# Performance work log

Measured on AMD Instinct MI355X. Metric: run time of the kernel, lower is better.

Reference implementation:

```python
import jax, jax.numpy as jnp
import numpy as np

B, T, C, HEAD = 8, 2048, 1024, 64


def setup_inputs() -> dict:
    key = jax.random.key(0)
    kx, kq, kk, kv = jax.random.split(key, 4)
    x = jax.random.normal(kx, (B, T, C), dtype=jnp.float32)
    Wq = jax.random.normal(kq, (C, HEAD), dtype=jnp.float32) * (C ** -0.5)
    Wk = jax.random.normal(kk, (C, HEAD), dtype=jnp.float32) * (C ** -0.5)
    Wv = jax.random.normal(kv, (C, HEAD), dtype=jnp.float32) * (C ** -0.5)
    return {"x": x, "Wq": Wq, "Wk": Wk, "Wv": Wv}


def reference(x, Wq, Wk, Wv):
    # q,k,v: [B, T, H] via bias-free linear projections
    q = jnp.einsum('btc,ch->bth', x, Wq)
    k = jnp.einsum('btc,ch->bth', x, Wk)
    v = jnp.einsum('btc,ch->bth', x, Wv)
    scale = k.shape[-1] ** -0.5
    # scores: [B, T, T]
    scores = jnp.einsum('bqh,bkh->bqk', q, k) * scale
    Tq = x.shape[1]
    causal = jnp.tril(jnp.ones((Tq, Tq), dtype=bool))  # [T, T]
    scores = jnp.where(causal[None, :, :], scores, -jnp.inf)
    # softmax forced to fp32 in the original (autocast block)
    weight = jax.nn.softmax(scores.astype(jnp.float32), axis=-1)
    # dropout is identity in eval / p=0 deterministic baseline
    out = jnp.einsum('bqk,bkh->bqh', weight.astype(v.dtype), v)  # [B, T, H]
    return out
```

## Files before the change

### kernel.cpp

```cpp
#include <hip/hip_runtime.h>
#include <hip/hip_bf16.h>
#include <stdint.h>

#define NB 8
#define NT 2048
#define NC 1024
#define NH 64

typedef __attribute__((ext_vector_type(8))) short bf16x8;
typedef __attribute__((ext_vector_type(4))) float f32x4;

#define MFMA(a, b, c) __builtin_amdgcn_mfma_f32_16x16x32_bf16((a), (b), (c), 0, 0, 0)

static __device__ __forceinline__ short f2bf(float f) {
  union { float f; uint32_t u; } v; v.f = f;
  uint32_t r = v.u + 0x7FFFu + ((v.u >> 16) & 1u);
  return (short)(r >> 16);
}
static __device__ __forceinline__ float bf2f(short h) {
  union { uint32_t u; float f; } v; v.u = ((uint32_t)(uint16_t)h) << 16;
  return v.f;
}
static __device__ __forceinline__ void gload_lds16(const void* g, void* l) {
  __builtin_amdgcn_global_load_lds(
      (const __attribute__((address_space(1))) uint32_t*)g,
      (__attribute__((address_space(3))) uint32_t*)l, 16, 0, 0);
}

__global__ __launch_bounds__(256) void w_prep(const float* __restrict__ Wq,
                                              const float* __restrict__ Wk,
                                              const float* __restrict__ Wv,
                                              short* __restrict__ Wt) {
  __shared__ short tile[64][68];
  const int blk = blockIdx.x;
  const int mat = blk / 16;
  const int k0 = (blk % 16) * 64;
  const float* W = (mat == 0) ? Wq : (mat == 1) ? Wk : Wv;
  const float scale = (mat == 0) ? 0.125f * 1.44269504088896f : 1.0f;
  const int tid = threadIdx.x;
  {
    int kk = tid >> 2;
    int h0 = (tid & 3) * 16;
    const float* src = W + (size_t)(k0 + kk) * NH + h0;
#pragma unroll
    for (int i = 0; i < 16; ++i) tile[kk][h0 + i] = f2bf(src[i] * scale);
  }
  __syncthreads();
  {
    int j = tid >> 2;
    int kk0 = (tid & 3) * 16;
    bf16x8 t0, t1;
#pragma unroll
    for (int i = 0; i < 8; ++i) { t0[i] = tile[kk0 + i][j]; t1[i] = tile[kk0 + 8 + i][j]; }
    short* dst = Wt + (size_t)(mat * 64 + j) * NC + k0 + kk0;
    *(bf16x8*)dst = t0;
    *(bf16x8*)(dst + 8) = t1;
  }
}

__global__ __launch_bounds__(512) void qkv_proj(const float* __restrict__ x,
                                                const short* __restrict__ Wt,
                                                short* __restrict__ Qo,
                                                short* __restrict__ Ko,
                                                short* __restrict__ VTo) {
  __shared__ char lds_raw[2][32768];
  const int tid = threadIdx.x;
  const int lane = tid & 63;
  const int wave = tid >> 6;
  const int l15 = lane & 15;
  const int hi = lane >> 4;
  const int m0 = blockIdx.x * 32;
  const int wr = wave & 1;
  const int wc = wave >> 1;

  f32x4 acc[3];
#pragma unroll
  for (int f = 0; f < 3; ++f) acc[f] = (f32x4){0.f, 0.f, 0.f, 0.f};

  int xr, xc;
  {
    int off = tid * 16;
    int ol = off ^ (((off >> 8) & 7) << 4);
    xr = ol >> 8; xc = (ol >> 2) & 63;
  }
  int wrow[3], wcol[3];
#pragma unroll
  for (int i = 0; i < 3; ++i) {
    int off = i * 8192 + tid * 16;
    int ol = off ^ (((off >> 7) & 7) << 4);
    wrow[i] = ol >> 7; wcol[i] = (ol >> 1) & 63;
  }

#define STAGE(k0, buf)                                                          \
  {                                                                             \
    char* xsb_ = lds_raw[buf];                                                  \
    char* wtb_ = lds_raw[buf] + 8192;                                           \
    gload_lds16(x + (size_t)(m0 + xr) * NC + (k0) + xc, xsb_ + tid * 16);       \
    _Pragma("unroll")                                                           \
    for (int i = 0; i < 3; ++i)                                                 \
      gload_lds16(Wt + (size_t)wrow[i] * NC + (k0) + wcol[i],                   \
                  wtb_ + i * 8192 + tid * 16);                                  \
  }

  STAGE(0, 0);
  __syncthreads();
  int cur = 0;
  for (int t = 0; t < 16; ++t) {
    if (t + 1 < 16) STAGE((t + 1) * 64, cur ^ 1);
    const char* xsb = lds_raw[cur];
    const char* wtb = lds_raw[cur] + 8192;
    const int r = wr * 16 + l15;
#pragma unroll
    for (int s = 0; s < 2; ++s) {
      int o1 = (r * 256 + s * 128 + hi * 32) ^ ((r & 7) << 4);
      int o2 = (r * 256 + s * 128 + hi * 32 + 16) ^ ((r & 7) << 4);
      float4 q0 = *(const float4*)(xsb + o1);
      float4 q1 = *(const float4*)(xsb + o2);
      bf16x8 a;
      a[0] = f2bf(q0.x); a[1] = f2bf(q0.y); a[2] = f2bf(q0.z); a[3] = f2bf(q0.w);
      a[4] = f2bf(q1.x); a[5] = f2bf(q1.y); a[6] = f2bf(q1.z); a[7] = f2bf(q1.w);
#pragma unroll
      for (int f = 0; f < 3; ++f) {
        int c = wc * 48 + f * 16 + l15;
        int ob = (c * 128 + s * 64 + hi * 16) ^ ((c & 7) << 4);
        bf16x8 b = *(const bf16x8*)(wtb + ob);
        acc[f] = MFMA(a, b, acc[f]);
      }
    }
    __syncthreads();
    cur ^= 1;
  }
#undef STAGE

#pragma unroll
  for (int f = 0; f < 3; ++f) {
    int c = wc * 48 + f * 16 + l15;
    int mat = c >> 6, h = c & 63;
    if (mat < 2) {
      short* dst = (mat == 0) ? Qo : Ko;
#pragma unroll
      for (int r = 0; r < 4; ++r) {
        int t = m0 + wr * 16 + hi * 4 + r;
        dst[(size_t)t * NH + h] = f2bf(acc[f][r]);
      }
    } else {
      int bb = m0 >> 11;
      int t0 = (m0 & 2047) + wr * 16 + hi * 4;
      short4 v;
      v.x = f2bf(acc[f][0]); v.y = f2bf(acc[f][1]);
      v.z = f2bf(acc[f][2]); v.w = f2bf(acc[f][3]);
      *(short4*)(VTo + ((size_t)(bb * 64 + h)) * NT + t0) = v;
    }
  }
}

__global__ __launch_bounds__(512, 2) void attn_fused(const short* __restrict__ Q,
                                                     const short* __restrict__ K,
                                                     const short* __restrict__ Vt,
                                                     float* __restrict__ out) {
  __shared__ short PO[8][32][72];
  __shared__ float Ls[8][32];

  const int tid = threadIdx.x;
  const int lane = tid & 63;
  const int wave = tid >> 6;
  const int l15 = lane & 15;
  const int hi = lane >> 4;
  const int kg = hi * 8;

  const int bid = blockIdx.x;
  const int half = bid >> 8;
  const int rr = bid & 255;
  const int b = rr >> 5;
  const int i = rr & 31;
  const int qt = (half == 0) ? (63 - i) : i;
  const int ktmax = qt >> 1;
  const int q0 = qt * 32;

  bf16x8 qf[2][2];
#pragma unroll
  for (int m = 0; m < 2; ++m)
#pragma unroll
    for (int s = 0; s < 2; ++s)
      qf[m][s] = *(const bf16x8*)(Q + ((size_t)b * NT + q0 + m * 16 + l15) * NH +
                                  s * 32 + kg);

  f32x4 oacc[2][4];
#pragma unroll
  for (int m = 0; m < 2; ++m)
#pragma unroll
    for (int f = 0; f < 4; ++f) oacc[m][f] = (f32x4){0.f, 0.f, 0.f, 0.f};
  float ps[2][4];
#pragma unroll
  for (int m = 0; m < 2; ++m)
#pragma unroll
    for (int r = 0; r < 4; ++r) ps[m][r] = 0.f;

#define LOAD_K(dst, kt_)                                                        \
  {                                                                             \
    const short* kb_ = K + ((size_t)b * NT + (kt_) * 64) * NH;                  \
    _Pragma("unroll") for (int n = 0; n < 4; ++n)                               \
    _Pragma("unroll") for (int s = 0; s < 2; ++s)                               \
      dst[n][s] = *(const bf16x8*)(kb_ + (n * 16 + l15) * NH + s * 32 + kg);    \
  }
#define LOAD_V(dst, kt_)                                                        \
  {                                                                             \
    _Pragma("unroll") for (int f = 0; f < 4; ++f)                               \
    _Pragma("unroll") for (int s = 0; s < 2; ++s)                               \
      dst[f][s] = *(const bf16x8*)(Vt + ((size_t)(b * 64 + f * 16 + l15)) * NT +\
                                   (kt_) * 64 + s * 32 + kg);                   \
  }

  int kt = wave;
  bf16x8 kf[4][2];
  if (kt <= ktmax) LOAD_K(kf, kt);

  for (; kt <= ktmax; kt += 8) {
    bf16x8 vf[4][2];
    LOAD_V(vf, kt);

    f32x4 S[2][4];
#pragma unroll
    for (int m = 0; m < 2; ++m)
#pragma unroll
      for (int n = 0; n < 4; ++n) {
        S[m][n] = (f32x4){0.f, 0.f, 0.f, 0.f};
        S[m][n] = MFMA(qf[m][0], kf[n][0], S[m][n]);
        S[m][n] = MFMA(qf[m][1], kf[n][1], S[m][n]);
      }

    bf16x8 kn[4][2];
    const bool more = (kt + 8) <= ktmax;
    if (more) LOAD_K(kn, kt + 8);

    if (kt == ktmax) {
#pragma unroll
      for (int m = 0; m < 2; ++m)
#pragma unroll
        for (int n = 0; n < 4; ++n)
#pragma unroll
          for (int r = 0; r < 4; ++r)
            if (kt * 64 + n * 16 + l15 > q0 + m * 16 + hi * 4 + r)
              S[m][n][r] = -INFINITY;
    }
#pragma unroll
    for (int m = 0; m < 2; ++m)
#pragma unroll
      for (int n = 0; n < 4; ++n)
#pragma unroll
        for (int r = 0; r < 4; ++r) {
          float p = __builtin_amdgcn_exp2f(S[m][n][r]);
          S[m][n][r] = p;
          ps[m][r] += p;
        }

#pragma unroll
    for (int m = 0; m < 2; ++m)
#pragma unroll
      for (int n = 0; n < 4; ++n)
#pragma unroll
        for (int r = 0; r < 4; ++r)
          PO[wave][m * 16 + hi * 4 + r][n * 16 + l15] = f2bf(S[m][n][r]);

    bf16x8 pa[2][2];
#pragma unroll
    for (int m = 0; m < 2; ++m)
#pragma unroll
      for (int s = 0; s < 2; ++s)
        pa[m][s] = *(const bf16x8*)&PO[wave][m * 16 + l15][s * 32 + kg];
#pragma unroll
    for (int m = 0; m < 2; ++m)
#pragma unroll
      for (int f = 0; f < 4; ++f) {
        oacc[m][f] = MFMA(pa[m][0], vf[f][0], oacc[m][f]);
        oacc[m][f] = MFMA(pa[m][1], vf[f][1], oacc[m][f]);
      }
    if (more) {
#pragma unroll
      for (int n = 0; n < 4; ++n)
#pragma unroll
        for (int s = 0; s < 2; ++s) kf[n][s] = kn[n][s];
    }
  }
#undef LOAD_K
#undef LOAD_V

#pragma unroll
  for (int d = 1; d < 16; d <<= 1)
#pragma unroll
    for (int m = 0; m < 2; ++m)
#pragma unroll
      for (int r = 0; r < 4; ++r) ps[m][r] += __shfl_xor(ps[m][r], d);

  if (l15 == 0) {
#pragma unroll
    for (int m = 0; m < 2; ++m)
#pragma unroll
      for (int r = 0; r < 4; ++r)
        Ls[wave][m * 16 + hi * 4 + r] = ps[m][r];
  }
#pragma unroll
  for (int m = 0; m < 2; ++m)
#pragma unroll
    for (int f = 0; f < 4; ++f)
#pragma unroll
      for (int r = 0; r < 4; ++r)
        PO[wave][m * 16 + hi * 4 + r][f * 16 + l15] = f2bf(oacc[m][f][r]);
  __syncthreads();

  {
    const int row = tid >> 4;
    const int c0 = (tid & 15) * 4;
    float L = 0.f;
    float o[4] = {0.f, 0.f, 0.f, 0.f};
#pragma unroll
    for (int w = 0; w < 8; ++w) {
      L += Ls[w][row];
      short4 v = *(const short4*)&PO[w][row][c0];
      o[0] += bf2f(v.x); o[1] += bf2f(v.y);
      o[2] += bf2f(v.z); o[3] += bf2f(v.w);
    }
    float inv = 1.f / L;
    float4 res = {o[0] * inv, o[1] * inv, o[2] * inv, o[3] * inv};
    *(float4*)(out + ((size_t)b * NT + q0 + row) * NH + c0) = res;
  }
}

extern "C" void kernel_launch(void* const* d_in, const int* in_sizes, int n_in,
                              void* d_out, int out_size, void* d_ws, size_t ws_size,
                              hipStream_t stream) {
  const float* x  = (const float*)d_in[0];
  const float* Wq = (const float*)d_in[1];
  const float* Wk = (const float*)d_in[2];
  const float* Wv = (const float*)d_in[3];
  float* out = (float*)d_out;

  char* ws = (char*)d_ws;
  short* Wt = (short*)ws;
  short* Qb = (short*)(ws + (size_t)(1 << 20));
  short* Kb = (short*)(ws + (size_t)(3 << 20));
  short* Vt = (short*)(ws + (size_t)(5 << 20));

  hipLaunchKernelGGL(w_prep, dim3(48), dim3(256), 0, stream, Wq, Wk, Wv, Wt);
  hipLaunchKernelGGL(qkv_proj, dim3(512), dim3(512), 0, stream, x, Wt, Qb, Kb, Vt);
  hipLaunchKernelGGL(attn_fused, dim3(512), dim3(512), 0, stream, Qb, Kb, Vt, out);
}
```

Baseline: 55.68 us.

## Shrink attention tile to 16 query rows with 4-wave blocks

New measurement: 61.02 us. +9.6%, slower.

```diff
diff --git a/kernel.cpp b/kernel.cpp
--- a/kernel.cpp
+++ b/kernel.cpp
@@ -154,12 +154,12 @@
   }
 }
 
-__global__ __launch_bounds__(512, 2) void attn_fused(const short* __restrict__ Q,
+__global__ __launch_bounds__(256, 4) void attn_fused(const short* __restrict__ Q,
                                                      const short* __restrict__ K,
                                                      const short* __restrict__ Vt,
                                                      float* __restrict__ out) {
-  __shared__ short PO[8][32][72];
-  __shared__ float Ls[8][32];
+  __shared__ short PO[4][16][72];
+  __shared__ float Ls[4][16];
 
   const int tid = threadIdx.x;
   const int lane = tid & 63;
@@ -169,143 +169,96 @@
   const int kg = hi * 8;
 
   const int bid = blockIdx.x;
-  const int half = bid >> 8;
-  const int rr = bid & 255;
-  const int b = rr >> 5;
-  const int i = rr & 31;
-  const int qt = (half == 0) ? (63 - i) : i;
-  const int ktmax = qt >> 1;
-  const int q0 = qt * 32;
-
-  bf16x8 qf[2][2];
-#pragma unroll
-  for (int m = 0; m < 2; ++m)
+  const int half = bid >> 9;
+  const int rr = bid & 511;
+  const int b = rr >> 6;
+  const int i = rr & 63;
+  const int qt = (half == 0) ? (127 - i) : i;
+  const int ktmax = qt >> 2;
+  const int q0 = qt * 16;
+
+  bf16x8 qf[2];
+#pragma unroll
+  for (int s = 0; s < 2; ++s)
+    qf[s] = *(const bf16x8*)(Q + ((size_t)b * NT + q0 + l15) * NH + s * 32 + kg);
+
+  f32x4 oacc[4];
+#pragma unroll
+  for (int f = 0; f < 4; ++f) oacc[f] = (f32x4){0.f, 0.f, 0.f, 0.f};
+  float ps[4];
+#pragma unroll
+  for (int r = 0; r < 4; ++r) ps[r] = 0.f;
+
+  for (int kt = wave; kt <= ktmax; kt += 4) {
+    const short* kb = K + ((size_t)b * NT + kt * 64) * NH;
+    bf16x8 kf[4][2], vf[4][2];
+#pragma unroll
+    for (int n = 0; n < 4; ++n)
+#pragma unroll
+      for (int s = 0; s < 2; ++s)
+        kf[n][s] = *(const bf16x8*)(kb + (n * 16 + l15) * NH + s * 32 + kg);
+#pragma unroll
+    for (int f = 0; f < 4; ++f)
+#pragma unroll
+      for (int s = 0; s < 2; ++s)
+        vf[f][s] = *(const bf16x8*)(Vt + ((size_t)(b * 64 + f * 16 + l15)) * NT +
+                                    kt * 64 + s * 32 + kg);
+
+    f32x4 S[4];
+#pragma unroll
+    for (int n = 0; n < 4; ++n) {
+      S[n] = (f32x4){0.f, 0.f, 0.f, 0.f};
+      S[n] = MFMA(qf[0], kf[n][0], S[n]);
+      S[n] = MFMA(qf[1], kf[n][1], S[n]);
+    }
+    if (kt == ktmax) {
+#pragma unroll
+      for (int n = 0; n < 4; ++n)
+#pragma unroll
+        for (int r = 0; r < 4; ++r)
+          if (kt * 64 + n * 16 + l15 > q0 + hi * 4 + r)
+            S[n][r] = -INFINITY;
+    }
+#pragma unroll
+    for (int n = 0; n < 4; ++n)
+#pragma unroll
+      for (int r = 0; r < 4; ++r) {
+        float p = __builtin_amdgcn_exp2f(S[n][r]);
+        S[n][r] = p;
+        ps[r] += p;
+      }
+
+#pragma unroll
+    for (int n = 0; n < 4; ++n)
+#pragma unroll
+      for (int r = 0; r < 4; ++r)
+        PO[wave][hi * 4 + r][n * 16 + l15] = f2bf(S[n][r]);
+
+    bf16x8 pa[2];
 #pragma unroll
     for (int s = 0; s < 2; ++s)
-      qf[m][s] = *(const bf16x8*)(Q + ((size_t)b * NT + q0 + m * 16 + l15) * NH +
-                                  s * 32 + kg);
-
-  f32x4 oacc[2][4];
-#pragma unroll
-  for (int m = 0; m < 2; ++m)
-#pragma unroll
-    for (int f = 0; f < 4; ++f) oacc[m][f] = (f32x4){0.f, 0.f, 0.f, 0.f};
-  float ps[2][4];
-#pragma unroll
-  for (int m = 0; m < 2; ++m)
-#pragma unroll
-    for (int r = 0; r < 4; ++r) ps[m][r] = 0.f;
-
-#define LOAD_K(dst, kt_)                                                        \
-  {                                                                             \
-    const short* kb_ = K + ((size_t)b * NT + (kt_) * 64) * NH;                  \
-    _Pragma("unroll") for (int n = 0; n < 4; ++n)                               \
-    _Pragma("unroll") for (int s = 0; s < 2; ++s)                               \
-      dst[n][s] = *(const bf16x8*)(kb_ + (n * 16 + l15) * NH + s * 32 + kg);    \
-  }
-#define LOAD_V(dst, kt_)                                                        \
-  {                                                                             \
-    _Pragma("unroll") for (int f = 0; f < 4; ++f)                               \
-    _Pragma("unroll") for (int s = 0; s < 2; ++s)                               \
-      dst[f][s] = *(const bf16x8*)(Vt + ((size_t)(b * 64 + f * 16 + l15)) * NT +\
-                                   (kt_) * 64 + s * 32 + kg);                   \
-  }
-
-  int kt = wave;
-  bf16x8 kf[4][2];
-  if (kt <= ktmax) LOAD_K(kf, kt);
-
-  for (; kt <= ktmax; kt += 8) {
-    bf16x8 vf[4][2];
-    LOAD_V(vf, kt);
-
-    f32x4 S[2][4];
-#pragma unroll
-    for (int m = 0; m < 2; ++m)
-#pragma unroll
-      for (int n = 0; n < 4; ++n) {
-        S[m][n] = (f32x4){0.f, 0.f, 0.f, 0.f};
-        S[m][n] = MFMA(qf[m][0], kf[n][0], S[m][n]);
-        S[m][n] = MFMA(qf[m][1], kf[n][1], S[m][n]);
-      }
-
-    bf16x8 kn[4][2];
-    const bool more = (kt + 8) <= ktmax;
-    if (more) LOAD_K(kn, kt + 8);
-
-    if (kt == ktmax) {
-#pragma unroll
-      for (int m = 0; m < 2; ++m)
-#pragma unroll
-        for (int n = 0; n < 4; ++n)
-#pragma unroll
-          for (int r = 0; r < 4; ++r)
-            if (kt * 64 + n * 16 + l15 > q0 + m * 16 + hi * 4 + r)
-              S[m][n][r] = -INFINITY;
-    }
-#pragma unroll
-    for (int m = 0; m < 2; ++m)
-#pragma unroll
-      for (int n = 0; n < 4; ++n)
-#pragma unroll
-        for (int r = 0; r < 4; ++r) {
-          float p = __builtin_amdgcn_exp2f(S[m][n][r]);
-          S[m][n][r] = p;
-          ps[m][r] += p;
-        }
-
-#pragma unroll
-    for (int m = 0; m < 2; ++m)
-#pragma unroll
-      for (int n = 0; n < 4; ++n)
-#pragma unroll
-        for (int r = 0; r < 4; ++r)
-          PO[wave][m * 16 + hi * 4 + r][n * 16 + l15] = f2bf(S[m][n][r]);
-
-    bf16x8 pa[2][2];
-#pragma unroll
-    for (int m = 0; m < 2; ++m)
-#pragma unroll
-      for (int s = 0; s < 2; ++s)
-        pa[m][s] = *(const bf16x8*)&PO[wave][m * 16 + l15][s * 32 + kg];
-#pragma unroll
-    for (int m = 0; m < 2; ++m)
-#pragma unroll
-      for (int f = 0; f < 4; ++f) {
-        oacc[m][f] = MFMA(pa[m][0], vf[f][0], oacc[m][f]);
-        oacc[m][f] = MFMA(pa[m][1], vf[f][1], oacc[m][f]);
-      }
-    if (more) {
-#pragma unroll
-      for (int n = 0; n < 4; ++n)
-#pragma unroll
-        for (int s = 0; s < 2; ++s) kf[n][s] = kn[n][s];
-    }
-  }
-#undef LOAD_K
-#undef LOAD_V
+      pa[s] = *(const bf16x8*)&PO[wave][l15][s * 32 + kg];
+#pragma unroll
+    for (int f = 0; f < 4; ++f) {
+      oacc[f] = MFMA(pa[0], vf[f][0], oacc[f]);
+      oacc[f] = MFMA(pa[1], vf[f][1], oacc[f]);
+    }
+  }
 
 #pragma unroll
   for (int d = 1; d < 16; d <<= 1)
 #pragma unroll
-    for (int m = 0; m < 2; ++m)
-#pragma unroll
-      for (int r = 0; r < 4; ++r) ps[m][r] += __shfl_xor(ps[m][r], d);
+    for (int r = 0; r < 4; ++r) ps[r] += __shfl_xor(ps[r], d);
 
   if (l15 == 0) {
 #pragma unroll
-    for (int m = 0; m < 2; ++m)
-#pragma unroll
-      for (int r = 0; r < 4; ++r)
-        Ls[wave][m * 16 + hi * 4 + r] = ps[m][r];
-  }
-#pragma unroll
-  for (int m = 0; m < 2; ++m)
-#pragma unroll
-    for (int f = 0; f < 4; ++f)
-#pragma unroll
-      for (int r = 0; r < 4; ++r)
-        PO[wave][m * 16 + hi * 4 + r][f * 16 + l15] = f2bf(oacc[m][f][r]);
+    for (int r = 0; r < 4; ++r) Ls[wave][hi * 4 + r] = ps[r];
+  }
+#pragma unroll
+  for (int f = 0; f < 4; ++f)
+#pragma unroll
+    for (int r = 0; r < 4; ++r)
+      PO[wave][hi * 4 + r][f * 16 + l15] = f2bf(oacc[f][r]);
   __syncthreads();
 
   {
@@ -314,7 +267,7 @@
     float L = 0.f;
     float o[4] = {0.f, 0.f, 0.f, 0.f};
 #pragma unroll
-    for (int w = 0; w < 8; ++w) {
+    for (int w = 0; w < 4; ++w) {
       L += Ls[w][row];
       short4 v = *(const short4*)&PO[w][row][c0];
       o[0] += bf2f(v.x); o[1] += bf2f(v.y);
@@ -343,5 +296,5 @@
 
   hipLaunchKernelGGL(w_prep, dim3(48), dim3(256), 0, stream, Wq, Wk, Wv, Wt);
   hipLaunchKernelGGL(qkv_proj, dim3(512), dim3(512), 0, stream, x, Wt, Qb, Kb, Vt);
-  hipLaunchKernelGGL(attn_fused, dim3(512), dim3(512), 0, stream, Qb, Kb, Vt, out);
-}
+  hipLaunchKernelGGL(attn_fused, dim3(1024), dim3(256), 0, stream, Qb, Kb, Vt, out);
+}
```
